# Kernel tuning notes

Hardware: AMD Instinct MI355X
Metric: run time of the kernel (lower is better)

## Reference

```python
import jax, jax.numpy as jnp
import numpy as np

ALPHA = 0.8
B = 32768

def setup_inputs() -> dict:
    key = jax.random.key(0)
    ks = jax.random.split(key, 18)
    def w(k, shape, fan_in):
        return (jax.random.normal(k, shape, dtype=jnp.float32) / np.sqrt(fan_in)).astype(jnp.float32)
    return {
        "f1_norm": jax.random.normal(ks[0], (B, 1, 768), dtype=jnp.float32),
        "f2_norm": jax.random.normal(ks[1], (B, 1, 600), dtype=jnp.float32),
        "W_enc1": w(ks[2], (64, 768), 768), "b_enc1": jnp.zeros((64,), jnp.float32),
        "W_enc2": w(ks[3], (64, 600), 600), "b_enc2": jnp.zeros((64,), jnp.float32),
        "W_aff_a": w(ks[4], (8, 2), 2), "W_aff_v": w(ks[5], (8, 2), 2),
        "W_a": w(ks[6], (32, 64), 64), "W_v": w(ks[7], (32, 64), 64),
        "W_ca": w(ks[8], (32, 8), 8), "W_cv": w(ks[9], (32, 8), 8),
        "W_ha": w(ks[10], (8, 32), 32), "W_hv": w(ks[11], (8, 32), 32),
        "W_r1": w(ks[12], (128, 1024), 1024), "b_r1": jnp.zeros((128,), jnp.float32),
        "W_r2": w(ks[13], (32, 128), 128), "b_r2": jnp.zeros((32,), jnp.float32),
    }

def reference(f1_norm, f2_norm, W_enc1, b_enc1, W_enc2, b_enc2,
              W_aff_a, W_aff_v, W_a, W_v, W_ca, W_cv, W_ha, W_hv,
              W_r1, b_r1, W_r2, b_r2):
    # Batched version of the per-sample loop. Per-sample: imu_fts [1,64], vis_fts [1,64].
    imu = f1_norm @ W_enc1.T + b_enc1            # [B,1,64]
    vis = f2_norm @ W_enc2.T + b_enc2            # [B,1,64]
    ivT = jnp.swapaxes(jnp.concatenate([imu, vis], axis=1), 1, 2)  # [B,64,2]
    a_t = ivT @ W_aff_a.T                        # [B,64,8]
    v_t = ivT @ W_aff_v.T                        # [B,64,8]
    scale = jnp.asarray(1.0 / 8.0, dtype=imu.dtype)  # 1/sqrt(64)
    imu_att = jnp.tanh((imu @ a_t) * scale)      # [B,1,8]
    vis_att = jnp.tanh((vis @ v_t) * scale)      # [B,1,8]
    H_a = jax.nn.relu(ALPHA * (imu_att @ W_ca.T + imu @ W_a.T))          # [B,1,32]
    H_v = jax.nn.relu((1.0 - ALPHA) * (vis_att @ W_cv.T + vis @ W_v.T))  # [B,1,32]
    # [B,8,1] + [B,1,64] broadcasts to [B,8,64] (matches torch broadcast in the loop)
    att_imu = ALPHA * jnp.swapaxes(H_a @ W_ha.T, 1, 2) + imu             # [B,8,64]
    att_vis = (1.0 - ALPHA) * jnp.swapaxes(H_v @ W_hv.T, 1, 2) + vis     # [B,8,64]
    feats = jnp.concatenate([att_imu, att_vis], axis=2).reshape(f1_norm.shape[0], 1024)
    h = feats @ W_r1.T + b_r1                    # [B,128]  (dropout = identity in eval)
    return h @ W_r2.T + b_r2                     # [B,32]
```

## Files before the change

kernel.cpp:

```cpp
#include <hip/hip_runtime.h>
#include <hip/hip_bf16.h>

#define ALPHA 0.8f
#define SPB 64
#define IVW 132

typedef __attribute__((ext_vector_type(8))) short bf16x8;
typedef __attribute__((ext_vector_type(8))) unsigned short ushort8;
typedef __attribute__((ext_vector_type(4))) float f32x4;

__device__ __host__ __forceinline__ unsigned short bfu(float x) {
    __hip_bfloat16 h = __float2bfloat16(x);
    return __builtin_bit_cast(unsigned short, h);
}

__global__ void prepA(const float* __restrict__ Wr1, float* __restrict__ M) {
    int idx = blockIdx.x * 256 + threadIdx.x;
    if (idx >= 144 * 128) return;
    int x = idx >> 7;
    int r = idx & 127;
    const float* row = Wr1 + (size_t)r * 1024;
    float s = 0.f;
    if (x < 64) {
        #pragma unroll
        for (int j = 0; j < 8; ++j) s += row[j * 128 + x];
    } else if (x < 128) {
        #pragma unroll
        for (int j = 0; j < 8; ++j) s += row[j * 128 + 64 + (x - 64)];
    } else if (x < 136) {
        int j = x - 128;
        for (int k = 0; k < 64; ++k) s += row[j * 128 + k];
    } else {
        int j = x - 136;
        for (int k = 0; k < 64; ++k) s += row[j * 128 + 64 + k];
    }
    M[x * 128 + r] = s;
}

__global__ void prepB(const float* __restrict__ M, const float* __restrict__ Wr2,
                      const float* __restrict__ br1, const float* __restrict__ br2,
                      float* __restrict__ G, float* __restrict__ c) {
    int idx = blockIdx.x * 256 + threadIdx.x;
    if (idx < 144 * 32) {
        int x = idx >> 5, o = idx & 31;
        const float* m = M + x * 128;
        const float* w = Wr2 + o * 128;
        float s = 0.f;
        for (int r = 0; r < 128; ++r) s = fmaf(m[r], w[r], s);
        G[x * 32 + o] = s;
    } else if (idx < 144 * 32 + 32) {
        int o = idx - 144 * 32;
        const float* w = Wr2 + o * 128;
        float s = br2[o];
        for (int r = 0; r < 128; ++r) s = fmaf(br1[r], w[r], s);
        c[o] = s;
    }
}

__global__ void prepW(const float* __restrict__ We1, const float* __restrict__ We2,
                      unsigned short* __restrict__ Wb1, unsigned short* __restrict__ Wb2) {
    int i = blockIdx.x * 256 + threadIdx.x;
    if (i < 64 * 768) Wb1[i] = bfu(We1[i]);
    if (i < 64 * 640) {
        int r = i / 640, k = i - r * 640;
        Wb2[i] = (k < 600) ? bfu(We2[r * 600 + k]) : (unsigned short)0;
    }
}

template <int ROWLEN, int KPAD, int KQ, int NCH>
__device__ __forceinline__ void encMF(const float* __restrict__ X,
                                      const unsigned short* __restrict__ Wb,
                                      const float* __restrict__ bias,
                                      short* sW, float* sIV,
                                      int colbase, int s0, int t) {
    const int w = t >> 6, l = t & 63;
    const int r16 = l & 15, kg = l >> 4;
    const float* xrow = X + (size_t)(s0 + w * 16 + r16) * ROWLEN;

    const int srow = t >> 2;
    const int sc0 = (t & 3) * 6;

    f32x4 acc0 = {0.f,0.f,0.f,0.f}, acc1 = {0.f,0.f,0.f,0.f};
    f32x4 acc2 = {0.f,0.f,0.f,0.f}, acc3 = {0.f,0.f,0.f,0.f};

    #pragma unroll
    for (int kq = 0; kq < 4; ++kq) {
        __syncthreads();
        const unsigned short* wsrc = Wb + srow * KPAD + kq * KQ;
        #pragma unroll
        for (int j = 0; j < 6; ++j) {
            const int c = sc0 + j;
            const int phys = (c & 24) | ((c & 7) ^ (srow & 7));
            ushort8 v;
            if (KQ == 192 || c < (KQ / 8)) {
                v = *(const ushort8*)(wsrc + c * 8);
            } else {
                #pragma unroll
                for (int e = 0; e < 8; ++e) v[e] = 0;
            }
            *(ushort8*)((char*)sW + srow * 384 + phys * 16) = v;
        }
        __syncthreads();

        #pragma unroll
        for (int kk = 0; kk < NCH; ++kk) {
            const int kb = kq * KQ + kk * 32 + kg * 8;
            ushort8 pa;
            #pragma unroll
            for (int e = 0; e < 8; ++e) pa[e] = 0;
            if (ROWLEN == KPAD || kb < ROWLEN) {
                const float4 u = *(const float4*)(xrow + kb);
                const float4 v2 = *(const float4*)(xrow + kb + 4);
                pa[0] = bfu(u.x); pa[1] = bfu(u.y); pa[2] = bfu(u.z); pa[3] = bfu(u.w);
                pa[4] = bfu(v2.x); pa[5] = bfu(v2.y); pa[6] = bfu(v2.z); pa[7] = bfu(v2.w);
            }
            const bf16x8 af = __builtin_bit_cast(bf16x8, pa);
            const int c = kk * 4 + kg;
            const int c24 = c & 24, c7 = c & 7;
            {
                const int n = r16;
                const bf16x8 bf = *(const bf16x8*)((const char*)sW + n * 384 + (c24 | (c7 ^ (n & 7))) * 16);
                acc0 = __builtin_amdgcn_mfma_f32_16x16x32_bf16(af, bf, acc0, 0, 0, 0);
            }
            {
                const int n = 16 + r16;
                const bf16x8 bf = *(const bf16x8*)((const char*)sW + n * 384 + (c24 | (c7 ^ (n & 7))) * 16);
                acc1 = __builtin_amdgcn_mfma_f32_16x16x32_bf16(af, bf, acc1, 0, 0, 0);
            }
            {
                const int n = 32 + r16;
                const bf16x8 bf = *(const bf16x8*)((const char*)sW + n * 384 + (c24 | (c7 ^ (n & 7))) * 16);
                acc2 = __builtin_amdgcn_mfma_f32_16x16x32_bf16(af, bf, acc2, 0, 0, 0);
            }
            {
                const int n = 48 + r16;
                const bf16x8 bf = *(const bf16x8*)((const char*)sW + n * 384 + (c24 | (c7 ^ (n & 7))) * 16);
                acc3 = __builtin_amdgcn_mfma_f32_16x16x32_bf16(af, bf, acc3, 0, 0, 0);
            }
        }
    }
    const int rr = 4 * kg;
    #pragma unroll
    for (int reg = 0; reg < 4; ++reg) {
        const int row = w * 16 + rr + reg;
        sIV[row * IVW + colbase +  0 + r16] = acc0[reg] + bias[ 0 + r16];
        sIV[row * IVW + colbase + 16 + r16] = acc1[reg] + bias[16 + r16];
        sIV[row * IVW + colbase + 32 + r16] = acc2[reg] + bias[32 + r16];
        sIV[row * IVW + colbase + 48 + r16] = acc3[reg] + bias[48 + r16];
    }
}

__global__ __launch_bounds__(256, 2)
void mica_main(const float* __restrict__ f1, const float* __restrict__ f2,
               const unsigned short* __restrict__ Wb1, const unsigned short* __restrict__ Wb2,
               const float* __restrict__ be1, const float* __restrict__ be2,
               const float* __restrict__ Waffa, const float* __restrict__ Waffv,
               const float* __restrict__ Wa, const float* __restrict__ Wv,
               const float* __restrict__ Wca, const float* __restrict__ Wcv,
               const float* __restrict__ Wha, const float* __restrict__ Whv,
               const float* __restrict__ G, const float* __restrict__ cvec,
               float* __restrict__ out) {
    __shared__ float sIV[SPB * IVW];
    __shared__ float scratch[6144];
    short* sW = (short*)scratch;
    const int t = threadIdx.x;
    const int s0 = blockIdx.x * SPB;

    encMF<768, 768, 192, 6>(f1, Wb1, be1, sW, sIV, 0, s0, t);
    encMF<600, 640, 160, 5>(f2, Wb2, be2, sW, sIV, 64, s0, t);
    __syncthreads();

    const int s = t & 63;
    const int q = t >> 6;
    const float* iv = sIV + s * IVW;
    float* red = scratch;

    float sii = 0.f, siv = 0.f, svv = 0.f;
    #pragma unroll
    for (int h = 0; h < 2; ++h) {
        const f32x4 a0 = *(const f32x4*)(iv + q * 16 + h * 8);
        const f32x4 a1 = *(const f32x4*)(iv + q * 16 + h * 8 + 4);
        const f32x4 b0 = *(const f32x4*)(iv + 64 + q * 16 + h * 8);
        const f32x4 b1 = *(const f32x4*)(iv + 64 + q * 16 + h * 8 + 4);
        #pragma unroll
        for (int j = 0; j < 4; ++j) {
            sii = fmaf(a0[j], a0[j], sii); siv = fmaf(a0[j], b0[j], siv); svv = fmaf(b0[j], b0[j], svv);
            sii = fmaf(a1[j], a1[j], sii); siv = fmaf(a1[j], b1[j], siv); svv = fmaf(b1[j], b1[j], svv);
        }
    }
    red[(q * 3 + 0) * 64 + s] = sii;
    red[(q * 3 + 1) * 64 + s] = siv;
    red[(q * 3 + 2) * 64 + s] = svv;
    __syncthreads();
    sii = 0.f; siv = 0.f; svv = 0.f;
    #pragma unroll
    for (int g = 0; g < 4; ++g) {
        sii += red[(g * 3 + 0) * 64 + s];
        siv += red[(g * 3 + 1) * 64 + s];
        svv += red[(g * 3 + 2) * 64 + s];
    }

    float ia[8], va[8];
    #pragma unroll
    for (int j = 0; j < 8; ++j) {
        ia[j] = tanhf((sii * Waffa[j * 2 + 0] + siv * Waffa[j * 2 + 1]) * 0.125f);
        va[j] = tanhf((siv * Waffv[j * 2 + 0] + svv * Waffv[j * 2 + 1]) * 0.125f);
    }

    float Ha[8], Hv[8];
    #pragma unroll
    for (int mi = 0; mi < 8; ++mi) {
        const int m = q * 8 + mi;
        float sa = 0.f, sv = 0.f;
        #pragma unroll
        for (int j = 0; j < 8; ++j) {
            sa = fmaf(ia[j], Wca[m * 8 + j], sa);
            sv = fmaf(va[j], Wcv[m * 8 + j], sv);
        }
        Ha[mi] = sa; Hv[mi] = sv;
    }
    for (int k4 = 0; k4 < 64; k4 += 4) {
        const f32x4 a4 = *(const f32x4*)(iv + k4);
        const f32x4 b4 = *(const f32x4*)(iv + 64 + k4);
        #pragma unroll
        for (int mi = 0; mi < 8; ++mi) {
            const int m = q * 8 + mi;
            const f32x4 wa = *(const f32x4*)(Wa + m * 64 + k4);
            const f32x4 wv = *(const f32x4*)(Wv + m * 64 + k4);
            #pragma unroll
            for (int j = 0; j < 4; ++j) {
                Ha[mi] = fmaf(a4[j], wa[j], Ha[mi]);
                Hv[mi] = fmaf(b4[j], wv[j], Hv[mi]);
            }
        }
    }
    #pragma unroll
    for (int mi = 0; mi < 8; ++mi) {
        Ha[mi] = fmaxf(ALPHA * Ha[mi], 0.f);
        Hv[mi] = fmaxf((1.f - ALPHA) * Hv[mi], 0.f);
    }

    __syncthreads();

    #pragma unroll
    for (int j = 0; j < 8; ++j) {
        float hap = 0.f, hvp = 0.f;
        #pragma unroll
        for (int mi = 0; mi < 8; ++mi) {
            hap = fmaf(Ha[mi], Wha[j * 32 + q * 8 + mi], hap);
            hvp = fmaf(Hv[mi], Whv[j * 32 + q * 8 + mi], hvp);
        }
        red[(q * 16 + j) * 64 + s] = hap;
        red[(q * 16 + 8 + j) * 64 + s] = hvp;
    }
    __syncthreads();
    float ha[8], hv[8];
    #pragma unroll
    for (int j = 0; j < 8; ++j) {
        float sa = 0.f, sv = 0.f;
        #pragma unroll
        for (int g = 0; g < 4; ++g) {
            sa += red[(g * 16 + j) * 64 + s];
            sv += red[(g * 16 + 8 + j) * 64 + s];
        }
        ha[j] = sa; hv[j] = sv;
    }

    float o8[8];
    #pragma unroll
    for (int oi = 0; oi < 8; ++oi) o8[oi] = cvec[q * 8 + oi];
    for (int k4 = 0; k4 < 128; k4 += 4) {
        const f32x4 a4 = *(const f32x4*)(iv + k4);
        #pragma unroll
        for (int kk = 0; kk < 4; ++kk) {
            const f32x4 g0 = *(const f32x4*)(G + (k4 + kk) * 32 + q * 8);
            const f32x4 g1 = *(const f32x4*)(G + (k4 + kk) * 32 + q * 8 + 4);
            #pragma unroll
            for (int oi = 0; oi < 4; ++oi) {
                o8[oi]     = fmaf(a4[kk], g0[oi], o8[oi]);
                o8[4 + oi] = fmaf(a4[kk], g1[oi], o8[4 + oi]);
            }
        }
    }
    #pragma unroll
    for (int j = 0; j < 8; ++j) {
        const float aj = ALPHA * ha[j];
        const float vj = (1.f - ALPHA) * hv[j];
        const f32x4 ga0 = *(const f32x4*)(G + (128 + j) * 32 + q * 8);
        const f32x4 ga1 = *(const f32x4*)(G + (128 + j) * 32 + q * 8 + 4);
        const f32x4 gv0 = *(const f32x4*)(G + (136 + j) * 32 + q * 8);
        const f32x4 gv1 = *(const f32x4*)(G + (136 + j) * 32 + q * 8 + 4);
        #pragma unroll
        for (int oi = 0; oi < 4; ++oi) {
            o8[oi]     = fmaf(aj, ga0[oi], o8[oi]);
            o8[4 + oi] = fmaf(aj, ga1[oi], o8[4 + oi]);
            o8[oi]     = fmaf(vj, gv0[oi], o8[oi]);
            o8[4 + oi] = fmaf(vj, gv1[oi], o8[4 + oi]);
        }
    }
    f32x4 v0 = {o8[0], o8[1], o8[2], o8[3]};
    f32x4 v1 = {o8[4], o8[5], o8[6], o8[7]};
    float* op = out + (size_t)(s0 + s) * 32 + q * 8;
    *(f32x4*)op = v0;
    *((f32x4*)op + 1) = v1;
}

extern "C" void kernel_launch(void* const* d_in, const int* in_sizes, int n_in,
                              void* d_out, int out_size, void* d_ws, size_t ws_size,
                              hipStream_t stream) {
    const float* f1    = (const float*)d_in[0];
    const float* f2    = (const float*)d_in[1];
    const float* We1   = (const float*)d_in[2];
    const float* be1   = (const float*)d_in[3];
    const float* We2   = (const float*)d_in[4];
    const float* be2   = (const float*)d_in[5];
    const float* Waffa = (const float*)d_in[6];
    const float* Waffv = (const float*)d_in[7];
    const float* Wa    = (const float*)d_in[8];
    const float* Wv    = (const float*)d_in[9];
    const float* Wca   = (const float*)d_in[10];
    const float* Wcv   = (const float*)d_in[11];
    const float* Wha   = (const float*)d_in[12];
    const float* Whv   = (const float*)d_in[13];
    const float* Wr1   = (const float*)d_in[14];
    const float* br1   = (const float*)d_in[15];
    const float* Wr2   = (const float*)d_in[16];
    const float* br2   = (const float*)d_in[17];
    float* outp = (float*)d_out;

    const int Btot = in_sizes[0] / 768;

    float* M = (float*)d_ws;
    float* G = (float*)((char*)d_ws + 73728);
    float* c = (float*)((char*)d_ws + 92160);
    unsigned short* Wb1 = (unsigned short*)((char*)d_ws + 92288);
    unsigned short* Wb2 = (unsigned short*)((char*)d_ws + 190592);

    prepA<<<(144 * 128 + 255) / 256, 256, 0, stream>>>(Wr1, M);
    prepB<<<(144 * 32 + 32 + 255) / 256, 256, 0, stream>>>(M, Wr2, br1, br2, G, c);
    prepW<<<(64 * 768 + 255) / 256, 256, 0, stream>>>(We1, We2, Wb1, Wb2);
    mica_main<<<Btot / SPB, 256, 0, stream>>>(f1, f2, Wb1, Wb2, be1, be2,
                                              Waffa, Waffv, Wa, Wv, Wca, Wcv, Wha, Whv,
                                              G, c, outp);
}
```

Measured before the change: 86.18 us.

## Split fused kernel into encoder and tail kernels with prepacked swizzled weights

Splits the fused kernel into two. An MFMA encoder kernel writes bf16 imu/vis features to a workspace buffer, and a separate per-sample tail kernel, using four threads per sample, reduces with shuffles instead of shared memory. Encoder weights are prepacked into the swizzled LDS layout so the staging loads are simple contiguous copies. The next K-chunk of activations is prefetched into registers while the current chunk is converted, and occupancy rises to four blocks per CU. The cost is a 16 MB bf16 round trip through global memory plus an extra launch, and the intermediate features lose precision to bf16.

```diff
diff --git a/kernel.cpp b/kernel.cpp
--- a/kernel.cpp
+++ b/kernel.cpp
@@ -9,9 +9,12 @@
 typedef __attribute__((ext_vector_type(8))) unsigned short ushort8;
 typedef __attribute__((ext_vector_type(4))) float f32x4;
 
-__device__ __host__ __forceinline__ unsigned short bfu(float x) {
+__device__ __forceinline__ unsigned short bfu(float x) {
     __hip_bfloat16 h = __float2bfloat16(x);
     return __builtin_bit_cast(unsigned short, h);
+}
+__device__ __forceinline__ float b2f(unsigned short u) {
+    return __builtin_bit_cast(float, ((unsigned)u) << 16);
 }
 
 __global__ void prepA(const float* __restrict__ Wr1, float* __restrict__ M) {
@@ -57,6 +60,274 @@
     }
 }
 
+__global__ void prepWpk(const float* __restrict__ We1, const float* __restrict__ We2,
+                        unsigned short* __restrict__ W1p, unsigned short* __restrict__ W2p) {
+    int idx = blockIdx.x * 256 + threadIdx.x;
+    if (idx >= 12288) return;
+    int enc = idx / 6144;
+    int ci = idx - enc * 6144;
+    int kq = ci / 1536;
+    int rem = ci % 1536;
+    int r = rem / 24, cch = rem % 24;
+    int phys = (cch & 24) | ((cch & 7) ^ (r & 7));
+    ushort8 v;
+    if (!enc) {
+        int k0 = kq * 192 + cch * 8;
+        #pragma unroll
+        for (int e = 0; e < 8; ++e) v[e] = bfu(We1[r * 768 + k0 + e]);
+        *(ushort8*)(W1p + kq * 12288 + r * 192 + phys * 8) = v;
+    } else {
+        int k0 = kq * 160 + cch * 8;
+        #pragma unroll
+        for (int e = 0; e < 8; ++e) {
+            int k = k0 + e;
+            v[e] = (cch < 20 && k < 600) ? bfu(We2[r * 600 + k]) : (unsigned short)0;
+        }
+        *(ushort8*)(W2p + kq * 12288 + r * 192 + phys * 8) = v;
+    }
+}
+
+template <int NCH, int KQ, int KLEN>
+__device__ __forceinline__ void encPk(const float* __restrict__ X,
+                                      const unsigned short* __restrict__ Wpk,
+                                      const float* __restrict__ bias,
+                                      short* sW, unsigned short* __restrict__ ivb,
+                                      int colbase, int s0, int t) {
+    const int w = t >> 6, l = t & 63;
+    const int r16 = l & 15, kg = l >> 4;
+    const float* xrow = X + (size_t)(s0 + w * 16 + r16) * KLEN;
+
+    f32x4 acc0 = {0.f,0.f,0.f,0.f}, acc1 = {0.f,0.f,0.f,0.f};
+    f32x4 acc2 = {0.f,0.f,0.f,0.f}, acc3 = {0.f,0.f,0.f,0.f};
+    f32x4 ra[2 * NCH];
+    ushort8 wr[6];
+
+    #pragma unroll
+    for (int kk = 0; kk < NCH; ++kk) {
+        const int kb = kk * 32 + kg * 8;
+        if (KLEN % 32 == 0 || kb + 8 <= KLEN) {
+            ra[2 * kk]     = *(const f32x4*)(xrow + kb);
+            ra[2 * kk + 1] = *(const f32x4*)(xrow + kb + 4);
+        } else {
+            ra[2 * kk] = f32x4{0.f,0.f,0.f,0.f};
+            ra[2 * kk + 1] = f32x4{0.f,0.f,0.f,0.f};
+        }
+    }
+
+    #pragma unroll
+    for (int kq = 0; kq < 4; ++kq) {
+        __syncthreads();
+        const unsigned short* wsrc = Wpk + kq * 12288 + t * 8;
+        #pragma unroll
+        for (int j = 0; j < 6; ++j) wr[j] = *(const ushort8*)(wsrc + j * 2048);
+        bf16x8 frag[NCH];
+        #pragma unroll
+        for (int kk = 0; kk < NCH; ++kk) {
+            ushort8 p;
+            #pragma unroll
+            for (int e = 0; e < 4; ++e) {
+                p[e]     = bfu(ra[2 * kk][e]);
+                p[4 + e] = bfu(ra[2 * kk + 1][e]);
+            }
+            frag[kk] = __builtin_bit_cast(bf16x8, p);
+        }
+        if (kq < 3) {
+            #pragma unroll
+            for (int kk = 0; kk < NCH; ++kk) {
+                const int kb = (kq + 1) * KQ + kk * 32 + kg * 8;
+                if (KLEN % 32 == 0 || kb + 8 <= KLEN) {
+                    ra[2 * kk]     = *(const f32x4*)(xrow + kb);
+                    ra[2 * kk + 1] = *(const f32x4*)(xrow + kb + 4);
+                } else {
+                    ra[2 * kk] = f32x4{0.f,0.f,0.f,0.f};
+                    ra[2 * kk + 1] = f32x4{0.f,0.f,0.f,0.f};
+                }
+            }
+        }
+        #pragma unroll
+        for (int j = 0; j < 6; ++j)
+            *(ushort8*)((char*)sW + (j * 256 + t) * 16) = wr[j];
+        __syncthreads();
+        #pragma unroll
+        for (int kk = 0; kk < NCH; ++kk) {
+            const int cch = kk * 4 + kg;
+            const int c24 = cch & 24, c7 = cch & 7;
+            const bf16x8 af = frag[kk];
+            {
+                const int n = r16;
+                const bf16x8 bf = *(const bf16x8*)((const char*)sW + n * 384 + (c24 | (c7 ^ (n & 7))) * 16);
+                acc0 = __builtin_amdgcn_mfma_f32_16x16x32_bf16(af, bf, acc0, 0, 0, 0);
+            }
+            {
+                const int n = 16 + r16;
+                const bf16x8 bf = *(const bf16x8*)((const char*)sW + n * 384 + (c24 | (c7 ^ (n & 7))) * 16);
+                acc1 = __builtin_amdgcn_mfma_f32_16x16x32_bf16(af, bf, acc1, 0, 0, 0);
+            }
+            {
+                const int n = 32 + r16;
+                const bf16x8 bf = *(const bf16x8*)((const char*)sW + n * 384 + (c24 | (c7 ^ (n & 7))) * 16);
+                acc2 = __builtin_amdgcn_mfma_f32_16x16x32_bf16(af, bf, acc2, 0, 0, 0);
+            }
+            {
+                const int n = 48 + r16;
+                const bf16x8 bf = *(const bf16x8*)((const char*)sW + n * 384 + (c24 | (c7 ^ (n & 7))) * 16);
+                acc3 = __builtin_amdgcn_mfma_f32_16x16x32_bf16(af, bf, acc3, 0, 0, 0);
+            }
+        }
+    }
+    const float bz0 = bias[r16], bz1 = bias[16 + r16], bz2 = bias[32 + r16], bz3 = bias[48 + r16];
+    const int rr = 4 * kg;
+    #pragma unroll
+    for (int reg = 0; reg < 4; ++reg) {
+        const size_t base = (size_t)(s0 + w * 16 + rr + reg) * 128 + colbase;
+        ivb[base +  0 + r16] = bfu(acc0[reg] + bz0);
+        ivb[base + 16 + r16] = bfu(acc1[reg] + bz1);
+        ivb[base + 32 + r16] = bfu(acc2[reg] + bz2);
+        ivb[base + 48 + r16] = bfu(acc3[reg] + bz3);
+    }
+}
+
+__global__ __launch_bounds__(256, 4)
+void mica_enc(const float* __restrict__ f1, const float* __restrict__ f2,
+              const unsigned short* __restrict__ W1p, const unsigned short* __restrict__ W2p,
+              const float* __restrict__ be1, const float* __restrict__ be2,
+              unsigned short* __restrict__ ivb) {
+    __shared__ __align__(16) short sW[12288];
+    const int t = threadIdx.x;
+    const int s0 = blockIdx.x * SPB;
+    encPk<6, 192, 768>(f1, W1p, be1, sW, ivb, 0,  s0, t);
+    encPk<5, 160, 600>(f2, W2p, be2, sW, ivb, 64, s0, t);
+}
+
+__global__ __launch_bounds__(256, 4)
+void mica_tail(const unsigned short* __restrict__ ivb,
+               const float* __restrict__ Waffa, const float* __restrict__ Waffv,
+               const float* __restrict__ Wa, const float* __restrict__ Wv,
+               const float* __restrict__ Wca, const float* __restrict__ Wcv,
+               const float* __restrict__ Wha, const float* __restrict__ Whv,
+               const float* __restrict__ G, const float* __restrict__ cvec,
+               float* __restrict__ out) {
+    const int gid = blockIdx.x * 256 + threadIdx.x;
+    const int s = gid >> 2, q = gid & 3;
+    const unsigned short* ivp = ivb + (size_t)s * 128;
+
+    ushort8 ivr[16];
+    #pragma unroll
+    for (int i = 0; i < 16; ++i) ivr[i] = *(const ushort8*)(ivp + i * 8);
+
+    float sii = 0.f, siv = 0.f, svv = 0.f;
+    #pragma unroll
+    for (int i = 0; i < 8; ++i) {
+        #pragma unroll
+        for (int e = 0; e < 8; ++e) {
+            const float a = b2f(ivr[i][e]), b = b2f(ivr[8 + i][e]);
+            sii = fmaf(a, a, sii); siv = fmaf(a, b, siv); svv = fmaf(b, b, svv);
+        }
+    }
+
+    float ia[8], va[8];
+    #pragma unroll
+    for (int j = 0; j < 8; ++j) {
+        ia[j] = tanhf((sii * Waffa[j * 2 + 0] + siv * Waffa[j * 2 + 1]) * 0.125f);
+        va[j] = tanhf((siv * Waffv[j * 2 + 0] + svv * Waffv[j * 2 + 1]) * 0.125f);
+    }
+
+    float Ha[8], Hv[8];
+    #pragma unroll
+    for (int mi = 0; mi < 8; ++mi) {
+        const int m = q * 8 + mi;
+        float sa = 0.f, sv = 0.f;
+        #pragma unroll
+        for (int j = 0; j < 8; ++j) {
+            sa = fmaf(ia[j], Wca[m * 8 + j], sa);
+            sv = fmaf(va[j], Wcv[m * 8 + j], sv);
+        }
+        Ha[mi] = sa; Hv[mi] = sv;
+    }
+    #pragma unroll
+    for (int i = 0; i < 8; ++i) {
+        float fa[8], fb[8];
+        #pragma unroll
+        for (int e = 0; e < 8; ++e) { fa[e] = b2f(ivr[i][e]); fb[e] = b2f(ivr[8 + i][e]); }
+        #pragma unroll
+        for (int mi = 0; mi < 8; ++mi) {
+            const int m = q * 8 + mi;
+            const f32x4 wa0 = *(const f32x4*)(Wa + m * 64 + i * 8);
+            const f32x4 wa1 = *(const f32x4*)(Wa + m * 64 + i * 8 + 4);
+            const f32x4 wv0 = *(const f32x4*)(Wv + m * 64 + i * 8);
+            const f32x4 wv1 = *(const f32x4*)(Wv + m * 64 + i * 8 + 4);
+            #pragma unroll
+            for (int e = 0; e < 4; ++e) {
+                Ha[mi] = fmaf(fa[e], wa0[e], Ha[mi]);
+                Ha[mi] = fmaf(fa[4 + e], wa1[e], Ha[mi]);
+                Hv[mi] = fmaf(fb[e], wv0[e], Hv[mi]);
+                Hv[mi] = fmaf(fb[4 + e], wv1[e], Hv[mi]);
+            }
+        }
+    }
+    #pragma unroll
+    for (int mi = 0; mi < 8; ++mi) {
+        Ha[mi] = fmaxf(ALPHA * Ha[mi], 0.f);
+        Hv[mi] = fmaxf((1.f - ALPHA) * Hv[mi], 0.f);
+    }
+
+    float ha[8], hv[8];
+    #pragma unroll
+    for (int j = 0; j < 8; ++j) {
+        float hap = 0.f, hvp = 0.f;
+        #pragma unroll
+        for (int mi = 0; mi < 8; ++mi) {
+            hap = fmaf(Ha[mi], Wha[j * 32 + q * 8 + mi], hap);
+            hvp = fmaf(Hv[mi], Whv[j * 32 + q * 8 + mi], hvp);
+        }
+        hap += __shfl_xor(hap, 1, 4); hap += __shfl_xor(hap, 2, 4);
+        hvp += __shfl_xor(hvp, 1, 4); hvp += __shfl_xor(hvp, 2, 4);
+        ha[j] = hap; hv[j] = hvp;
+    }
+
+    float o8[8];
+    #pragma unroll
+    for (int oi = 0; oi < 8; ++oi) o8[oi] = cvec[q * 8 + oi];
+    #pragma unroll
+    for (int i = 0; i < 16; ++i) {
+        float fx[8];
+        #pragma unroll
+        for (int e = 0; e < 8; ++e) fx[e] = b2f(ivr[i][e]);
+        #pragma unroll
+        for (int e = 0; e < 8; ++e) {
+            const int k = i * 8 + e;
+            const f32x4 g0 = *(const f32x4*)(G + k * 32 + q * 8);
+            const f32x4 g1 = *(const f32x4*)(G + k * 32 + q * 8 + 4);
+            #pragma unroll
+            for (int oi = 0; oi < 4; ++oi) {
+                o8[oi]     = fmaf(fx[e], g0[oi], o8[oi]);
+                o8[4 + oi] = fmaf(fx[e], g1[oi], o8[4 + oi]);
+            }
+        }
+    }
+    #pragma unroll
+    for (int j = 0; j < 8; ++j) {
+        const float aj = ALPHA * ha[j];
+        const float vj = (1.f - ALPHA) * hv[j];
+        const f32x4 ga0 = *(const f32x4*)(G + (128 + j) * 32 + q * 8);
+        const f32x4 ga1 = *(const f32x4*)(G + (128 + j) * 32 + q * 8 + 4);
+        const f32x4 gv0 = *(const f32x4*)(G + (136 + j) * 32 + q * 8);
+        const f32x4 gv1 = *(const f32x4*)(G + (136 + j) * 32 + q * 8 + 4);
+        #pragma unroll
+        for (int oi = 0; oi < 4; ++oi) {
+            o8[oi]     = fmaf(aj, ga0[oi], o8[oi]);
+            o8[4 + oi] = fmaf(aj, ga1[oi], o8[4 + oi]);
+            o8[oi]     = fmaf(vj, gv0[oi], o8[oi]);
+            o8[4 + oi] = fmaf(vj, gv1[oi], o8[4 + oi]);
+        }
+    }
+    f32x4 v0 = {o8[0], o8[1], o8[2], o8[3]};
+    f32x4 v1 = {o8[4], o8[5], o8[6], o8[7]};
+    float* op = out + (size_t)s * 32 + q * 8;
+    *(f32x4*)op = v0;
+    *((f32x4*)op + 1) = v1;
+}
+
 __global__ void prepW(const float* __restrict__ We1, const float* __restrict__ We2,
                       unsigned short* __restrict__ Wb1, unsigned short* __restrict__ Wb2) {
     int i = blockIdx.x * 256 + threadIdx.x;
@@ -76,13 +347,10 @@
     const int w = t >> 6, l = t & 63;
     const int r16 = l & 15, kg = l >> 4;
     const float* xrow = X + (size_t)(s0 + w * 16 + r16) * ROWLEN;
-
     const int srow = t >> 2;
     const int sc0 = (t & 3) * 6;
-
     f32x4 acc0 = {0.f,0.f,0.f,0.f}, acc1 = {0.f,0.f,0.f,0.f};
     f32x4 acc2 = {0.f,0.f,0.f,0.f}, acc3 = {0.f,0.f,0.f,0.f};
-
     #pragma unroll
     for (int kq = 0; kq < 4; ++kq) {
         __syncthreads();
@@ -95,13 +363,11 @@
             if (KQ == 192 || c < (KQ / 8)) {
                 v = *(const ushort8*)(wsrc + c * 8);
             } else {
-                #pragma unroll
                 for (int e = 0; e < 8; ++e) v[e] = 0;
             }
             *(ushort8*)((char*)sW + srow * 384 + phys * 16) = v;
         }
         __syncthreads();
-
         #pragma unroll
         for (int kk = 0; kk < NCH; ++kk) {
             const int kb = kq * KQ + kk * 32 + kg * 8;
@@ -165,16 +431,13 @@
     short* sW = (short*)scratch;
     const int t = threadIdx.x;
     const int s0 = blockIdx.x * SPB;
-
     encMF<768, 768, 192, 6>(f1, Wb1, be1, sW, sIV, 0, s0, t);
     encMF<600, 640, 160, 5>(f2, Wb2, be2, sW, sIV, 64, s0, t);
     __syncthreads();
-
     const int s = t & 63;
     const int q = t >> 6;
     const float* iv = sIV + s * IVW;
     float* red = scratch;
-
     float sii = 0.f, siv = 0.f, svv = 0.f;
     #pragma unroll
     for (int h = 0; h < 2; ++h) {
@@ -199,14 +462,12 @@
         siv += red[(g * 3 + 1) * 64 + s];
         svv += red[(g * 3 + 2) * 64 + s];
     }
-
     float ia[8], va[8];
     #pragma unroll
     for (int j = 0; j < 8; ++j) {
         ia[j] = tanhf((sii * Waffa[j * 2 + 0] + siv * Waffa[j * 2 + 1]) * 0.125f);
         va[j] = tanhf((siv * Waffv[j * 2 + 0] + svv * Waffv[j * 2 + 1]) * 0.125f);
     }
-
     float Ha[8], Hv[8];
     #pragma unroll
     for (int mi = 0; mi < 8; ++mi) {
@@ -239,9 +500,7 @@
         Ha[mi] = fmaxf(ALPHA * Ha[mi], 0.f);
         Hv[mi] = fmaxf((1.f - ALPHA) * Hv[mi], 0.f);
     }
-
     __syncthreads();
-
     #pragma unroll
     for (int j = 0; j < 8; ++j) {
         float hap = 0.f, hvp = 0.f;
@@ -265,7 +524,6 @@
         }
         ha[j] = sa; hv[j] = sv;
     }
-
     float o8[8];
     #pragma unroll
     for (int oi = 0; oi < 8; ++oi) o8[oi] = cvec[q * 8 + oi];
@@ -333,13 +591,25 @@
     float* M = (float*)d_ws;
     float* G = (float*)((char*)d_ws + 73728);
     float* c = (float*)((char*)d_ws + 92160);
-    unsigned short* Wb1 = (unsigned short*)((char*)d_ws + 92288);
-    unsigned short* Wb2 = (unsigned short*)((char*)d_ws + 190592);
 
     prepA<<<(144 * 128 + 255) / 256, 256, 0, stream>>>(Wr1, M);
     prepB<<<(144 * 32 + 32 + 255) / 256, 256, 0, stream>>>(M, Wr2, br1, br2, G, c);
-    prepW<<<(64 * 768 + 255) / 256, 256, 0, stream>>>(We1, We2, Wb1, Wb2);
-    mica_main<<<Btot / SPB, 256, 0, stream>>>(f1, f2, Wb1, Wb2, be1, be2,
-                                              Waffa, Waffv, Wa, Wv, Wca, Wcv, Wha, Whv,
-                                              G, c, outp);
-}
+
+    const size_t need = 288896 + (size_t)Btot * 256;
+    if (ws_size >= need) {
+        unsigned short* W1p = (unsigned short*)((char*)d_ws + 92288);
+        unsigned short* W2p = (unsigned short*)((char*)d_ws + 190592);
+        unsigned short* ivb = (unsigned short*)((char*)d_ws + 288896);
+        prepWpk<<<48, 256, 0, stream>>>(We1, We2, W1p, W2p);
+        mica_enc<<<Btot / SPB, 256, 0, stream>>>(f1, f2, W1p, W2p, be1, be2, ivb);
+        mica_tail<<<(Btot * 4) / 256, 256, 0, stream>>>(ivb, Waffa, Waffv, Wa, Wv,
+                                                        Wca, Wcv, Wha, Whv, G, c, outp);
+    } else {
+        unsigned short* Wb1 = (unsigned short*)((char*)d_ws + 92288);
+        unsigned short* Wb2 = (unsigned short*)((char*)d_ws + 190592);
+        prepW<<<(64 * 768 + 255) / 256, 256, 0, stream>>>(We1, We2, Wb1, Wb2);
+        mica_main<<<Btot / SPB, 256, 0, stream>>>(f1, f2, Wb1, Wb2, be1, be2,
+                                                  Waffa, Waffv, Wa, Wv, Wca, Wcv, Wha, Whv,
+                                                  G, c, outp);
+    }
+}
```

Result: slower. 220.5 us (+155.8%).

## Split encoder into separate kernel with prepacked swizzled weights and register prefetch

Applied to the files above, without the earlier changes.

Splits the fused kernel into an encoder kernel and a tail kernel, handing the 128 encoder features per sample between them as bf16 in a global workspace. The encoder kernel uses less LDS so it can take higher occupancy (launch bounds of 4). The encoder weights are now pre-swizzled in a prep kernel, so each tile is staged into LDS with plain contiguous copies. Input rows are prefetched into registers one K-chunk ahead to overlap global loads with MFMA work. In exchange it adds a global round-trip for the intermediate features, an extra kernel launch, and bf16 rounding of the encoder outputs before the attention tail.

```diff
diff --git a/kernel.cpp b/kernel.cpp
--- a/kernel.cpp
+++ b/kernel.cpp
@@ -9,9 +9,12 @@
 typedef __attribute__((ext_vector_type(8))) unsigned short ushort8;
 typedef __attribute__((ext_vector_type(4))) float f32x4;
 
-__device__ __host__ __forceinline__ unsigned short bfu(float x) {
+__device__ __forceinline__ unsigned short bfu(float x) {
     __hip_bfloat16 h = __float2bfloat16(x);
     return __builtin_bit_cast(unsigned short, h);
+}
+__device__ __forceinline__ float b2f(unsigned short u) {
+    return __builtin_bit_cast(float, ((unsigned)u) << 16);
 }
 
 __global__ void prepA(const float* __restrict__ Wr1, float* __restrict__ M) {
@@ -57,66 +60,99 @@
     }
 }
 
-__global__ void prepW(const float* __restrict__ We1, const float* __restrict__ We2,
-                      unsigned short* __restrict__ Wb1, unsigned short* __restrict__ Wb2) {
-    int i = blockIdx.x * 256 + threadIdx.x;
-    if (i < 64 * 768) Wb1[i] = bfu(We1[i]);
-    if (i < 64 * 640) {
-        int r = i / 640, k = i - r * 640;
-        Wb2[i] = (k < 600) ? bfu(We2[r * 600 + k]) : (unsigned short)0;
-    }
-}
-
-template <int ROWLEN, int KPAD, int KQ, int NCH>
-__device__ __forceinline__ void encMF(const float* __restrict__ X,
-                                      const unsigned short* __restrict__ Wb,
+__global__ void prepWpk(const float* __restrict__ We1, const float* __restrict__ We2,
+                        unsigned short* __restrict__ W1p, unsigned short* __restrict__ W2p) {
+    int idx = blockIdx.x * 256 + threadIdx.x;
+    if (idx >= 12288) return;
+    int enc = idx / 6144;
+    int ci = idx - enc * 6144;
+    int kq = ci / 1536;
+    int rem = ci % 1536;
+    int r = rem / 24, cch = rem % 24;
+    int phys = (cch & 24) | ((cch & 7) ^ (r & 7));
+    ushort8 v;
+    if (!enc) {
+        int k0 = kq * 192 + cch * 8;
+        #pragma unroll
+        for (int e = 0; e < 8; ++e) v[e] = bfu(We1[r * 768 + k0 + e]);
+        *(ushort8*)(W1p + kq * 12288 + r * 192 + phys * 8) = v;
+    } else {
+        int k0 = kq * 160 + cch * 8;
+        #pragma unroll
+        for (int e = 0; e < 8; ++e) {
+            int k = k0 + e;
+            v[e] = (cch < 20 && k < 600) ? bfu(We2[r * 600 + k]) : (unsigned short)0;
+        }
+        *(ushort8*)(W2p + kq * 12288 + r * 192 + phys * 8) = v;
+    }
+}
+
+template <int NCH, int KQ, int KLEN>
+__device__ __forceinline__ void encPk(const float* __restrict__ X,
+                                      const unsigned short* __restrict__ Wpk,
                                       const float* __restrict__ bias,
-                                      short* sW, float* sIV,
+                                      short* sW, unsigned short* __restrict__ ivb,
                                       int colbase, int s0, int t) {
     const int w = t >> 6, l = t & 63;
     const int r16 = l & 15, kg = l >> 4;
-    const float* xrow = X + (size_t)(s0 + w * 16 + r16) * ROWLEN;
-
-    const int srow = t >> 2;
-    const int sc0 = (t & 3) * 6;
+    const float* xrow = X + (size_t)(s0 + w * 16 + r16) * KLEN;
 
     f32x4 acc0 = {0.f,0.f,0.f,0.f}, acc1 = {0.f,0.f,0.f,0.f};
     f32x4 acc2 = {0.f,0.f,0.f,0.f}, acc3 = {0.f,0.f,0.f,0.f};
+    f32x4 ra[2 * NCH];
+    ushort8 wr[6];
+
+    #pragma unroll
+    for (int kk = 0; kk < NCH; ++kk) {
+        const int kb = kk * 32 + kg * 8;
+        if (KLEN % 32 == 0 || kb + 8 <= KLEN) {
+            ra[2 * kk]     = *(const f32x4*)(xrow + kb);
+            ra[2 * kk + 1] = *(const f32x4*)(xrow + kb + 4);
+        } else {
+            ra[2 * kk] = f32x4{0.f,0.f,0.f,0.f};
+            ra[2 * kk + 1] = f32x4{0.f,0.f,0.f,0.f};
+        }
+    }
 
     #pragma unroll
     for (int kq = 0; kq < 4; ++kq) {
         __syncthreads();
-        const unsigned short* wsrc = Wb + srow * KPAD + kq * KQ;
-        #pragma unroll
-        for (int j = 0; j < 6; ++j) {
-            const int c = sc0 + j;
-            const int phys = (c & 24) | ((c & 7) ^ (srow & 7));
-            ushort8 v;
-            if (KQ == 192 || c < (KQ / 8)) {
-                v = *(const ushort8*)(wsrc + c * 8);
-            } else {
-                #pragma unroll
-                for (int e = 0; e < 8; ++e) v[e] = 0;
-            }
-            *(ushort8*)((char*)sW + srow * 384 + phys * 16) = v;
-        }
+        const unsigned short* wsrc = Wpk + kq * 12288 + t * 8;
+        #pragma unroll
+        for (int j = 0; j < 6; ++j) wr[j] = *(const ushort8*)(wsrc + j * 2048);
+        bf16x8 frag[NCH];
+        #pragma unroll
+        for (int kk = 0; kk < NCH; ++kk) {
+            ushort8 p;
+            #pragma unroll
+            for (int e = 0; e < 4; ++e) {
+                p[e]     = bfu(ra[2 * kk][e]);
+                p[4 + e] = bfu(ra[2 * kk + 1][e]);
+            }
+            frag[kk] = __builtin_bit_cast(bf16x8, p);
+        }
+        if (kq < 3) {
+            #pragma unroll
+            for (int kk = 0; kk < NCH; ++kk) {
+                const int kb = (kq + 1) * KQ + kk * 32 + kg * 8;
+                if (KLEN % 32 == 0 || kb + 8 <= KLEN) {
+                    ra[2 * kk]     = *(const f32x4*)(xrow + kb);
+                    ra[2 * kk + 1] = *(const f32x4*)(xrow + kb + 4);
+                } else {
+                    ra[2 * kk] = f32x4{0.f,0.f,0.f,0.f};
+                    ra[2 * kk + 1] = f32x4{0.f,0.f,0.f,0.f};
+                }
+            }
+        }
+        #pragma unroll
+        for (int j = 0; j < 6; ++j)
+            *(ushort8*)((char*)sW + (j * 256 + t) * 16) = wr[j];
         __syncthreads();
-
         #pragma unroll
         for (int kk = 0; kk < NCH; ++kk) {
-            const int kb = kq * KQ + kk * 32 + kg * 8;
-            ushort8 pa;
-            #pragma unroll
-            for (int e = 0; e < 8; ++e) pa[e] = 0;
-            if (ROWLEN == KPAD || kb < ROWLEN) {
-                const float4 u = *(const float4*)(xrow + kb);
-                const float4 v2 = *(const float4*)(xrow + kb + 4);
-                pa[0] = bfu(u.x); pa[1] = bfu(u.y); pa[2] = bfu(u.z); pa[3] = bfu(u.w);
-                pa[4] = bfu(v2.x); pa[5] = bfu(v2.y); pa[6] = bfu(v2.z); pa[7] = bfu(v2.w);
-            }
-            const bf16x8 af = __builtin_bit_cast(bf16x8, pa);
-            const int c = kk * 4 + kg;
-            const int c24 = c & 24, c7 = c & 7;
+            const int cch = kk * 4 + kg;
+            const int c24 = cch & 24, c7 = cch & 7;
+            const bf16x8 af = frag[kk];
             {
                 const int n = r16;
                 const bf16x8 bf = *(const bf16x8*)((const char*)sW + n * 384 + (c24 | (c7 ^ (n & 7))) * 16);
@@ -139,21 +175,32 @@
             }
         }
     }
+    const float bz0 = bias[r16], bz1 = bias[16 + r16], bz2 = bias[32 + r16], bz3 = bias[48 + r16];
     const int rr = 4 * kg;
     #pragma unroll
     for (int reg = 0; reg < 4; ++reg) {
-        const int row = w * 16 + rr + reg;
-        sIV[row * IVW + colbase +  0 + r16] = acc0[reg] + bias[ 0 + r16];
-        sIV[row * IVW + colbase + 16 + r16] = acc1[reg] + bias[16 + r16];
-        sIV[row * IVW + colbase + 32 + r16] = acc2[reg] + bias[32 + r16];
-        sIV[row * IVW + colbase + 48 + r16] = acc3[reg] + bias[48 + r16];
-    }
+        const size_t base = (size_t)(s0 + w * 16 + rr + reg) * 128 + colbase;
+        ivb[base +  0 + r16] = bfu(acc0[reg] + bz0);
+        ivb[base + 16 + r16] = bfu(acc1[reg] + bz1);
+        ivb[base + 32 + r16] = bfu(acc2[reg] + bz2);
+        ivb[base + 48 + r16] = bfu(acc3[reg] + bz3);
+    }
+}
+
+__global__ __launch_bounds__(256, 4)
+void mica_enc(const float* __restrict__ f1, const float* __restrict__ f2,
+              const unsigned short* __restrict__ W1p, const unsigned short* __restrict__ W2p,
+              const float* __restrict__ be1, const float* __restrict__ be2,
+              unsigned short* __restrict__ ivb) {
+    __shared__ __align__(16) short sW[12288];
+    const int t = threadIdx.x;
+    const int s0 = blockIdx.x * SPB;
+    encPk<6, 192, 768>(f1, W1p, be1, sW, ivb, 0,  s0, t);
+    encPk<5, 160, 600>(f2, W2p, be2, sW, ivb, 64, s0, t);
 }
 
 __global__ __launch_bounds__(256, 2)
-void mica_main(const float* __restrict__ f1, const float* __restrict__ f2,
-               const unsigned short* __restrict__ Wb1, const unsigned short* __restrict__ Wb2,
-               const float* __restrict__ be1, const float* __restrict__ be2,
+void mica_tail(const unsigned short* __restrict__ ivb,
                const float* __restrict__ Waffa, const float* __restrict__ Waffv,
                const float* __restrict__ Wa, const float* __restrict__ Wv,
                const float* __restrict__ Wca, const float* __restrict__ Wcv,
@@ -161,19 +208,27 @@
                const float* __restrict__ G, const float* __restrict__ cvec,
                float* __restrict__ out) {
     __shared__ float sIV[SPB * IVW];
-    __shared__ float scratch[6144];
-    short* sW = (short*)scratch;
+    __shared__ float red[4096];
     const int t = threadIdx.x;
     const int s0 = blockIdx.x * SPB;
 
-    encMF<768, 768, 192, 6>(f1, Wb1, be1, sW, sIV, 0, s0, t);
-    encMF<600, 640, 160, 5>(f2, Wb2, be2, sW, sIV, 64, s0, t);
+    {
+        const int row = t & 63, cb = (t >> 6) * 32;
+        const unsigned short* src = ivb + (size_t)(s0 + row) * 128 + cb;
+        #pragma unroll
+        for (int j = 0; j < 4; ++j) {
+            const ushort8 v = *(const ushort8*)(src + j * 8);
+            f32x4 f0 = {b2f(v[0]), b2f(v[1]), b2f(v[2]), b2f(v[3])};
+            f32x4 f1 = {b2f(v[4]), b2f(v[5]), b2f(v[6]), b2f(v[7])};
+            *(f32x4*)(sIV + row * IVW + cb + j * 8)     = f0;
+            *(f32x4*)(sIV + row * IVW + cb + j * 8 + 4) = f1;
+        }
+    }
     __syncthreads();
 
     const int s = t & 63;
     const int q = t >> 6;
     const float* iv = sIV + s * IVW;
-    float* red = scratch;
 
     float sii = 0.f, siv = 0.f, svv = 0.f;
     #pragma unroll
@@ -333,13 +388,14 @@
     float* M = (float*)d_ws;
     float* G = (float*)((char*)d_ws + 73728);
     float* c = (float*)((char*)d_ws + 92160);
-    unsigned short* Wb1 = (unsigned short*)((char*)d_ws + 92288);
-    unsigned short* Wb2 = (unsigned short*)((char*)d_ws + 190592);
+    unsigned short* W1p = (unsigned short*)((char*)d_ws + 92288);
+    unsigned short* W2p = (unsigned short*)((char*)d_ws + 190592);
+    unsigned short* ivb = (unsigned short*)((char*)d_ws + 288896);
 
     prepA<<<(144 * 128 + 255) / 256, 256, 0, stream>>>(Wr1, M);
     prepB<<<(144 * 32 + 32 + 255) / 256, 256, 0, stream>>>(M, Wr2, br1, br2, G, c);
-    prepW<<<(64 * 768 + 255) / 256, 256, 0, stream>>>(We1, We2, Wb1, Wb2);
-    mica_main<<<Btot / SPB, 256, 0, stream>>>(f1, f2, Wb1, Wb2, be1, be2,
-                                              Waffa, Waffv, Wa, Wv, Wca, Wcv, Wha, Whv,
-                                              G, c, outp);
-}
+    prepWpk<<<48, 256, 0, stream>>>(We1, We2, W1p, W2p);
+    mica_enc<<<Btot / SPB, 256, 0, stream>>>(f1, f2, W1p, W2p, be1, be2, ivb);
+    mica_tail<<<Btot / SPB, 256, 0, stream>>>(ivb, Waffa, Waffv, Wa, Wv,
+                                              Wca, Wcv, Wha, Whv, G, c, outp);
+}
```

Result: slower. 91.80 us (median of 2 runs) (+6.5%).

## Split encoder and tail into separate kernels, read encoder weights directly from global

Applied to the files above, without the earlier changes.

The fused kernel becomes two kernels. The encoder kernel no longer stages weights through LDS with barriers: it loads bf16 weight fragments straight from global/L2 and writes bf16 encoder outputs to a workspace buffer. A second kernel reads those outputs back, converts them to fp32 in LDS and runs the attention/regression tail. This drops LDS staging and the barriers in the encoder loop, at the cost of an extra global round trip, a kernel launch, and bf16 rounding of the intermediate features.

```diff
diff --git a/kernel.cpp b/kernel.cpp
--- a/kernel.cpp
+++ b/kernel.cpp
@@ -9,9 +9,12 @@
 typedef __attribute__((ext_vector_type(8))) unsigned short ushort8;
 typedef __attribute__((ext_vector_type(4))) float f32x4;
 
-__device__ __host__ __forceinline__ unsigned short bfu(float x) {
+__device__ __forceinline__ unsigned short bfu(float x) {
     __hip_bfloat16 h = __float2bfloat16(x);
     return __builtin_bit_cast(unsigned short, h);
+}
+__device__ __forceinline__ float b2f(unsigned short u) {
+    return __builtin_bit_cast(float, ((unsigned)u) << 16);
 }
 
 __global__ void prepA(const float* __restrict__ Wr1, float* __restrict__ M) {
@@ -67,93 +70,71 @@
     }
 }
 
-template <int ROWLEN, int KPAD, int KQ, int NCH>
-__device__ __forceinline__ void encMF(const float* __restrict__ X,
+template <int NCH, int KPAD, int KLEN>
+__device__ __forceinline__ void encNB(const float* __restrict__ X,
                                       const unsigned short* __restrict__ Wb,
                                       const float* __restrict__ bias,
-                                      short* sW, float* sIV,
+                                      unsigned short* __restrict__ ivb,
                                       int colbase, int s0, int t) {
     const int w = t >> 6, l = t & 63;
     const int r16 = l & 15, kg = l >> 4;
-    const float* xrow = X + (size_t)(s0 + w * 16 + r16) * ROWLEN;
-
-    const int srow = t >> 2;
-    const int sc0 = (t & 3) * 6;
+    const float* xrow = X + (size_t)(s0 + w * 16 + r16) * KLEN;
+    const unsigned short* wbA = Wb + (size_t)( 0 + r16) * KPAD;
+    const unsigned short* wbB = Wb + (size_t)(16 + r16) * KPAD;
+    const unsigned short* wbC = Wb + (size_t)(32 + r16) * KPAD;
+    const unsigned short* wbD = Wb + (size_t)(48 + r16) * KPAD;
 
     f32x4 acc0 = {0.f,0.f,0.f,0.f}, acc1 = {0.f,0.f,0.f,0.f};
     f32x4 acc2 = {0.f,0.f,0.f,0.f}, acc3 = {0.f,0.f,0.f,0.f};
 
-    #pragma unroll
-    for (int kq = 0; kq < 4; ++kq) {
-        __syncthreads();
-        const unsigned short* wsrc = Wb + srow * KPAD + kq * KQ;
-        #pragma unroll
-        for (int j = 0; j < 6; ++j) {
-            const int c = sc0 + j;
-            const int phys = (c & 24) | ((c & 7) ^ (srow & 7));
-            ushort8 v;
-            if (KQ == 192 || c < (KQ / 8)) {
-                v = *(const ushort8*)(wsrc + c * 8);
-            } else {
-                #pragma unroll
-                for (int e = 0; e < 8; ++e) v[e] = 0;
-            }
-            *(ushort8*)((char*)sW + srow * 384 + phys * 16) = v;
-        }
-        __syncthreads();
-
-        #pragma unroll
-        for (int kk = 0; kk < NCH; ++kk) {
-            const int kb = kq * KQ + kk * 32 + kg * 8;
-            ushort8 pa;
-            #pragma unroll
-            for (int e = 0; e < 8; ++e) pa[e] = 0;
-            if (ROWLEN == KPAD || kb < ROWLEN) {
-                const float4 u = *(const float4*)(xrow + kb);
-                const float4 v2 = *(const float4*)(xrow + kb + 4);
-                pa[0] = bfu(u.x); pa[1] = bfu(u.y); pa[2] = bfu(u.z); pa[3] = bfu(u.w);
-                pa[4] = bfu(v2.x); pa[5] = bfu(v2.y); pa[6] = bfu(v2.z); pa[7] = bfu(v2.w);
-            }
-            const bf16x8 af = __builtin_bit_cast(bf16x8, pa);
-            const int c = kk * 4 + kg;
-            const int c24 = c & 24, c7 = c & 7;
-            {
-                const int n = r16;
-                const bf16x8 bf = *(const bf16x8*)((const char*)sW + n * 384 + (c24 | (c7 ^ (n & 7))) * 16);
-                acc0 = __builtin_amdgcn_mfma_f32_16x16x32_bf16(af, bf, acc0, 0, 0, 0);
-            }
-            {
-                const int n = 16 + r16;
-                const bf16x8 bf = *(const bf16x8*)((const char*)sW + n * 384 + (c24 | (c7 ^ (n & 7))) * 16);
-                acc1 = __builtin_amdgcn_mfma_f32_16x16x32_bf16(af, bf, acc1, 0, 0, 0);
-            }
-            {
-                const int n = 32 + r16;
-                const bf16x8 bf = *(const bf16x8*)((const char*)sW + n * 384 + (c24 | (c7 ^ (n & 7))) * 16);
-                acc2 = __builtin_amdgcn_mfma_f32_16x16x32_bf16(af, bf, acc2, 0, 0, 0);
-            }
-            {
-                const int n = 48 + r16;
-                const bf16x8 bf = *(const bf16x8*)((const char*)sW + n * 384 + (c24 | (c7 ^ (n & 7))) * 16);
-                acc3 = __builtin_amdgcn_mfma_f32_16x16x32_bf16(af, bf, acc3, 0, 0, 0);
-            }
-        }
-    }
+    #pragma unroll 4
+    for (int kk = 0; kk < NCH; ++kk) {
+        const int kb = kk * 32 + kg * 8;
+        ushort8 pa;
+        #pragma unroll
+        for (int e = 0; e < 8; ++e) pa[e] = 0;
+        if (KPAD == KLEN || kb + 8 <= KLEN) {
+            const f32x4 u = *(const f32x4*)(xrow + kb);
+            const f32x4 v = *(const f32x4*)(xrow + kb + 4);
+            pa[0] = bfu(u[0]); pa[1] = bfu(u[1]); pa[2] = bfu(u[2]); pa[3] = bfu(u[3]);
+            pa[4] = bfu(v[0]); pa[5] = bfu(v[1]); pa[6] = bfu(v[2]); pa[7] = bfu(v[3]);
+        }
+        const bf16x8 af = __builtin_bit_cast(bf16x8, pa);
+        const bf16x8 b0 = *(const bf16x8*)(wbA + kb);
+        const bf16x8 b1 = *(const bf16x8*)(wbB + kb);
+        const bf16x8 b2 = *(const bf16x8*)(wbC + kb);
+        const bf16x8 b3 = *(const bf16x8*)(wbD + kb);
+        acc0 = __builtin_amdgcn_mfma_f32_16x16x32_bf16(af, b0, acc0, 0, 0, 0);
+        acc1 = __builtin_amdgcn_mfma_f32_16x16x32_bf16(af, b1, acc1, 0, 0, 0);
+        acc2 = __builtin_amdgcn_mfma_f32_16x16x32_bf16(af, b2, acc2, 0, 0, 0);
+        acc3 = __builtin_amdgcn_mfma_f32_16x16x32_bf16(af, b3, acc3, 0, 0, 0);
+    }
+
+    const float bz0 = bias[r16], bz1 = bias[16 + r16], bz2 = bias[32 + r16], bz3 = bias[48 + r16];
     const int rr = 4 * kg;
     #pragma unroll
     for (int reg = 0; reg < 4; ++reg) {
-        const int row = w * 16 + rr + reg;
-        sIV[row * IVW + colbase +  0 + r16] = acc0[reg] + bias[ 0 + r16];
-        sIV[row * IVW + colbase + 16 + r16] = acc1[reg] + bias[16 + r16];
-        sIV[row * IVW + colbase + 32 + r16] = acc2[reg] + bias[32 + r16];
-        sIV[row * IVW + colbase + 48 + r16] = acc3[reg] + bias[48 + r16];
+        const size_t base = (size_t)(s0 + w * 16 + rr + reg) * 128 + colbase;
+        ivb[base +  0 + r16] = bfu(acc0[reg] + bz0);
+        ivb[base + 16 + r16] = bfu(acc1[reg] + bz1);
+        ivb[base + 32 + r16] = bfu(acc2[reg] + bz2);
+        ivb[base + 48 + r16] = bfu(acc3[reg] + bz3);
     }
 }
 
 __global__ __launch_bounds__(256, 2)
-void mica_main(const float* __restrict__ f1, const float* __restrict__ f2,
-               const unsigned short* __restrict__ Wb1, const unsigned short* __restrict__ Wb2,
-               const float* __restrict__ be1, const float* __restrict__ be2,
+void mica_enc(const float* __restrict__ f1, const float* __restrict__ f2,
+              const unsigned short* __restrict__ Wb1, const unsigned short* __restrict__ Wb2,
+              const float* __restrict__ be1, const float* __restrict__ be2,
+              unsigned short* __restrict__ ivb) {
+    const int t = threadIdx.x;
+    const int s0 = blockIdx.x * SPB;
+    encNB<24, 768, 768>(f1, Wb1, be1, ivb, 0,  s0, t);
+    encNB<20, 640, 600>(f2, Wb2, be2, ivb, 64, s0, t);
+}
+
+__global__ __launch_bounds__(256, 2)
+void mica_tail(const unsigned short* __restrict__ ivb,
                const float* __restrict__ Waffa, const float* __restrict__ Waffv,
                const float* __restrict__ Wa, const float* __restrict__ Wv,
                const float* __restrict__ Wca, const float* __restrict__ Wcv,
@@ -161,19 +142,27 @@
                const float* __restrict__ G, const float* __restrict__ cvec,
                float* __restrict__ out) {
     __shared__ float sIV[SPB * IVW];
-    __shared__ float scratch[6144];
-    short* sW = (short*)scratch;
+    __shared__ float red[4096];
     const int t = threadIdx.x;
     const int s0 = blockIdx.x * SPB;
 
-    encMF<768, 768, 192, 6>(f1, Wb1, be1, sW, sIV, 0, s0, t);
-    encMF<600, 640, 160, 5>(f2, Wb2, be2, sW, sIV, 64, s0, t);
+    {
+        const int row = t & 63, cb = (t >> 6) * 32;
+        const unsigned short* src = ivb + (size_t)(s0 + row) * 128 + cb;
+        #pragma unroll
+        for (int j = 0; j < 4; ++j) {
+            const ushort8 v = *(const ushort8*)(src + j * 8);
+            f32x4 f0 = {b2f(v[0]), b2f(v[1]), b2f(v[2]), b2f(v[3])};
+            f32x4 f1 = {b2f(v[4]), b2f(v[5]), b2f(v[6]), b2f(v[7])};
+            *(f32x4*)(sIV + row * IVW + cb + j * 8)     = f0;
+            *(f32x4*)(sIV + row * IVW + cb + j * 8 + 4) = f1;
+        }
+    }
     __syncthreads();
 
     const int s = t & 63;
     const int q = t >> 6;
     const float* iv = sIV + s * IVW;
-    float* red = scratch;
 
     float sii = 0.f, siv = 0.f, svv = 0.f;
     #pragma unroll
@@ -335,11 +324,12 @@
     float* c = (float*)((char*)d_ws + 92160);
     unsigned short* Wb1 = (unsigned short*)((char*)d_ws + 92288);
     unsigned short* Wb2 = (unsigned short*)((char*)d_ws + 190592);
+    unsigned short* ivb = (unsigned short*)((char*)d_ws + 272512);
 
     prepA<<<(144 * 128 + 255) / 256, 256, 0, stream>>>(Wr1, M);
     prepB<<<(144 * 32 + 32 + 255) / 256, 256, 0, stream>>>(M, Wr2, br1, br2, G, c);
     prepW<<<(64 * 768 + 255) / 256, 256, 0, stream>>>(We1, We2, Wb1, Wb2);
-    mica_main<<<Btot / SPB, 256, 0, stream>>>(f1, f2, Wb1, Wb2, be1, be2,
-                                              Waffa, Waffv, Wa, Wv, Wca, Wcv, Wha, Whv,
-                                              G, c, outp);
-}
+    mica_enc<<<Btot / SPB, 256, 0, stream>>>(f1, f2, Wb1, Wb2, be1, be2, ivb);
+    mica_tail<<<Btot / SPB, 256, 0, stream>>>(ivb, Waffa, Waffv, Wa, Wv,
+                                              Wca, Wcv, Wha, Whv, G, c, outp);
+}
```

Measured after the change: 114.9 us. +33.3%, slower.
